# Kernel tuning notes

Measured on AMD Instinct MI355X. Metric: run time of the kernel, lower is better.

Reference implementation:

```python
import jax, jax.numpy as jnp
import numpy as np

WIN = 7
N = WIN * WIN  # 49 tokens per window
C = 384
H = 12
HD = C // H
B_ = 4096
NW = 64  # number of distinct window masks; must divide B_


def _relative_position_index(wh=WIN, ww=WIN):
    coords = np.stack(np.meshgrid(np.arange(wh), np.arange(ww), indexing='ij'))  # [2,wh,ww]
    cf = coords.reshape(2, -1)
    rel = cf[:, :, None] - cf[:, None, :]               # [2,N,N]
    rel = rel.transpose(1, 2, 0).astype(np.int32)       # [N,N,2]
    rel[:, :, 0] += wh - 1
    rel[:, :, 1] += ww - 1
    rel[:, :, 0] *= 2 * ww - 1
    return jnp.asarray(rel.sum(-1))                     # [N,N] int32


def setup_inputs() -> dict:
    key = jax.random.key(0)
    ks = jax.random.split(key, 8)
    std = 0.02
    return {
        'x': jax.random.normal(ks[0], (B_, N, C), jnp.float32),
        'mask': jnp.zeros((NW, N, N), jnp.float32),  # 0/-inf mask; zeros here
        'qkv_w': jax.random.normal(ks[1], (3 * C, C), jnp.float32) * std,
        'qkv_b': jnp.zeros((3 * C,), jnp.float32),
        'rpb_table': jax.random.normal(ks[2], ((2 * WIN - 1) ** 2, H), jnp.float32) * std,
        'proj_l_w': jax.random.normal(ks[3], (H, H), jnp.float32) * std,
        'proj_l_b': jnp.zeros((H,), jnp.float32),
        'proj_w_w': jax.random.normal(ks[4], (H, H), jnp.float32) * std,
        'proj_w_b': jnp.zeros((H,), jnp.float32),
        'proj_weight': jax.random.normal(ks[5], (C, C), jnp.float32) * std,
        'proj_bias': jnp.zeros((C,), jnp.float32),
        'rel_index': _relative_position_index(),
    }


def reference(x, mask, qkv_w, qkv_b, rpb_table, proj_l_w, proj_l_b,
              proj_w_w, proj_w_b, proj_weight, proj_bias, rel_index):
    B, n, c = x.shape
    scale = HD ** (-0.5)
    qkv = x @ qkv_w.T + qkv_b                     # [B,N,3C]
    q_out, k_out, v_out = jnp.split(qkv, 3, axis=-1)  # each [B,N,C]
    qkv5 = qkv.reshape(B, n, 3, H, HD)
    q = qkv5[:, :, 0].transpose(0, 2, 1, 3)       # [B,H,N,hd]
    k = qkv5[:, :, 1].transpose(0, 2, 1, 3)
    v = qkv5[:, :, 2].transpose(0, 2, 1, 3)
    attn = jnp.einsum('bhnd,bhmd->bhnm', q * scale, k)   # [B,H,N,N]
    bias = rpb_table[rel_index]                   # [N,N,H]
    attn = attn + bias.transpose(2, 0, 1)[None]
    # proj_l: linear mixing across heads (Linear acts on last dim after permute)
    attn = jnp.einsum('bhnm,gh->bgnm', attn, proj_l_w) + proj_l_b[None, :, None, None]
    nW = mask.shape[0]
    attn = attn.reshape(B // nW, nW, H, n, n) + mask[None, :, None]
    attn = attn.reshape(B, H, n, n)
    attn = jax.nn.softmax(attn, axis=-1)
    # proj_w: head mixing after softmax
    attn = jnp.einsum('bhnm,gh->bgnm', attn, proj_w_w) + proj_w_b[None, :, None, None]
    out = jnp.einsum('bhnm,bhmd->bnhd', attn, v).reshape(B, n, c)
    out = out @ proj_weight.T + proj_bias
    return (out, (q_out, k_out, v_out))
```

## Files before the change

### kernel.cpp

```cpp
#include <hip/hip_runtime.h>
#include <hip/hip_bf16.h>

#define TOK 49
#define NPT 2401
#define CDIM 384
#define NH 12
#define HDIM 32
#define NWIN 64
#define BTOT 4096
#define OUTSZ (BTOT * TOK * CDIM)
#define L2E 1.4426950408889634f

typedef __attribute__((ext_vector_type(8))) short bf16x8;
typedef __attribute__((ext_vector_type(4))) float f32x4;
typedef unsigned int uint32;
typedef unsigned short ushort_t;

__device__ inline ushort_t f2bf(float f) {
  uint32 u = __float_as_uint(f);
  u += 0x7FFF + ((u >> 16) & 1);
  return (ushort_t)(u >> 16);
}
__device__ inline uint32 pk2(float a, float b) {
  union { __hip_bfloat162 h; uint32 u; } x;
  x.h = __float22bfloat162_rn(float2{a, b});
  return x.u;
}
__device__ inline float bf2f(uint32 u) { return __uint_as_float((u & 0xffffu) << 16); }
__device__ inline bf16x8 pack8(float4 a, float4 b) {
  union { __hip_bfloat162 h[4]; bf16x8 v; } u;
  u.h[0] = __float22bfloat162_rn(float2{a.x, a.y});
  u.h[1] = __float22bfloat162_rn(float2{a.z, a.w});
  u.h[2] = __float22bfloat162_rn(float2{b.x, b.y});
  u.h[3] = __float22bfloat162_rn(float2{b.z, b.w});
  return u.v;
}
__device__ inline bf16x8 pack8f(const float* f) {
  union { __hip_bfloat162 h[4]; bf16x8 v; } u;
#pragma unroll
  for (int i = 0; i < 4; ++i) u.h[i] = __float22bfloat162_rn(float2{f[2*i], f[2*i+1]});
  return u.v;
}

__global__ void k_cvt(const float* __restrict__ src, ushort_t* __restrict__ dst, int n8) {
  int i = blockIdx.x * 256 + threadIdx.x;
  if (i >= n8) return;
  const float4* s = (const float4*)(src + (size_t)i * 8);
  float4 a = s[0], b = s[1];
  uint4 o;
  o.x = (uint32)f2bf(a.x) | ((uint32)f2bf(a.y) << 16);
  o.y = (uint32)f2bf(a.z) | ((uint32)f2bf(a.w) << 16);
  o.z = (uint32)f2bf(b.x) | ((uint32)f2bf(b.y) << 16);
  o.w = (uint32)f2bf(b.z) | ((uint32)f2bf(b.w) << 16);
  *(uint4*)(dst + (size_t)i * 8) = o;
}

__global__ void k_bias2(const float* __restrict__ rpb, const float* __restrict__ plw,
                        const float* __restrict__ plb, const int* __restrict__ relidx,
                        ushort_t* __restrict__ bmf) {
  int i = blockIdx.x * 256 + threadIdx.x;
  if (i >= NPT * 12) return;
  int p = i / 12, g = i - (i / 12) * 12;
  int rid = relidx[p];
  float s = plb[g];
#pragma unroll
  for (int h = 0; h < NH; ++h) s = fmaf(plw[g * NH + h], rpb[rid * NH + h], s);
  bmf[i] = f2bf(s * L2E);
}

__global__ void k_bias3(const float* __restrict__ rpb, const float* __restrict__ plw,
                        const float* __restrict__ plb, const int* __restrict__ relidx,
                        const float* __restrict__ mask, ushort_t* __restrict__ bmfw) {
  int i = blockIdx.x * 256 + threadIdx.x;
  if (i >= NWIN * NPT * 12) return;
  int w = i / (NPT * 12);
  int rem = i - w * (NPT * 12);
  int p = rem / 12, g = rem - (rem / 12) * 12;
  int rid = relidx[p];
  float s = plb[g];
#pragma unroll
  for (int h = 0; h < NH; ++h) s = fmaf(plw[g * NH + h], rpb[rid * NH + h], s);
  bmfw[i] = f2bf((s + mask[w * NPT + p]) * L2E);
}

__launch_bounds__(256)
__global__ void k_qkv_mfma(const ushort_t* __restrict__ Xb, const ushort_t* __restrict__ Wb,
                           const float* __restrict__ Bq, float* __restrict__ qslab) {
  __shared__ __align__(16) ushort_t As[128 * 64];
  __shared__ __align__(16) ushort_t Bs[128 * 64];
  const int bid = blockIdx.x;
  const int sw = (bid & 7) * 1764 + (bid >> 3);
  const int bx = sw / 9;
  const int by = sw - bx * 9;
  const int tid = threadIdx.x;
  const int l = tid & 63, l15 = l & 15, l16 = l >> 4;
  const int wv = tid >> 6;
  const int wr = wv >> 1, wc = wv & 1;
  const int row0 = bx * 128;
  const int col0 = by * 128;

  f32x4 acc[4][4];
#pragma unroll
  for (int i = 0; i < 4; ++i)
#pragma unroll
    for (int j = 0; j < 4; ++j)
#pragma unroll
      for (int e = 0; e < 4; ++e) acc[i][j][e] = 0.f;

  const int sr = tid >> 3, sc = tid & 7;
  const int sidx = (sr * 64 + sc * 8) ^ ((sr & 7) << 3);

  for (int kb = 0; kb < CDIM; kb += 64) {
#pragma unroll
    for (int i = 0; i < 4; ++i) {
      int r = sr + i * 32;
      int idx = (sidx + i * 32 * 64) ^ 0;
      uint4 v = *(const uint4*)&Xb[(size_t)(row0 + r) * CDIM + kb + sc * 8];
      *(uint4*)&As[idx] = v;
      uint4 w = *(const uint4*)&Wb[(size_t)(col0 + r) * CDIM + kb + sc * 8];
      *(uint4*)&Bs[idx] = w;
    }
    __syncthreads();
#pragma unroll
    for (int ks = 0; ks < 2; ++ks) {
      bf16x8 af[4], bfr[4];
#pragma unroll
      for (int mt = 0; mt < 4; ++mt) {
        int row = wr * 64 + mt * 16 + l15;
        af[mt] = *(const bf16x8*)&As[(row * 64 + ks * 32 + l16 * 8) ^ ((row & 7) << 3)];
      }
#pragma unroll
      for (int nt = 0; nt < 4; ++nt) {
        int row = wc * 64 + nt * 16 + l15;
        bfr[nt] = *(const bf16x8*)&Bs[(row * 64 + ks * 32 + l16 * 8) ^ ((row & 7) << 3)];
      }
#pragma unroll
      for (int mt = 0; mt < 4; ++mt)
#pragma unroll
        for (int nt = 0; nt < 4; ++nt)
          acc[mt][nt] = __builtin_amdgcn_mfma_f32_16x16x32_bf16(af[mt], bfr[nt], acc[mt][nt], 0, 0, 0);
    }
    __syncthreads();
  }

  const int slab = by / 3;
  const int cslab0 = col0 - slab * CDIM;
  float* dst = qslab + (size_t)slab * OUTSZ;
#pragma unroll
  for (int nt = 0; nt < 4; ++nt) {
    int colg = col0 + wc * 64 + nt * 16 + l15;
    int colo = cslab0 + wc * 64 + nt * 16 + l15;
    float bv = Bq[colg];
#pragma unroll
    for (int mt = 0; mt < 4; ++mt) {
      int rbase = row0 + wr * 64 + mt * 16 + l16 * 4;
#pragma unroll
      for (int j = 0; j < 4; ++j)
        dst[(size_t)(rbase + j) * CDIM + colo] = acc[mt][nt][j] + bv;
    }
  }
}

__launch_bounds__(1024, 8)
__global__ void k_attn9(const float* __restrict__ qslab, const float* __restrict__ kslab,
                        const float* __restrict__ vslab, const float* __restrict__ mask,
                        const ushort_t* __restrict__ bmf, int wstride,
                        const float* __restrict__ plw, const float* __restrict__ pww,
                        const float* __restrict__ pwb, float* __restrict__ xout) {
  __shared__ __align__(16) ushort_t SA[19976];
  __shared__ __align__(16) ushort_t PP[12 * 1400 + 416];

  const int tid = threadIdx.x;
  const int b  = blockIdx.x >> 1;
  const int bh = blockIdx.x & 1;
  const int n0 = bh * 25;
  const int NR = bh ? 24 : 25;
  const size_t base = (size_t)b * TOK * CDIM;
  const int l = tid & 63, l15 = l & 15, l16 = l >> 4;
  const int wv = tid >> 6;
  const float SCL = 0.17677669529663687f * L2E;

  for (int p = tid; p < 1240; p += 1024) *(uint2*)&SA[p * 16 + 12] = uint2{0u, 0u};
  if (tid < 580) *(uint32*)&SA[18816 + tid * 2] = 0u;
  if (tid < 208) *(uint32*)&PP[12 * 1400 + tid * 2] = 0u;

  {
    const int art = wv >> 3;
    const int act = (wv >> 1) & 3;
    const int ah0 = (wv & 1) * 6;
    const int nrow = art * 16 + l15;
    const int mrow = act * 16 + l15;
    const bool qv = nrow < NR;
    const bool kv = mrow < TOK;
#pragma unroll
    for (int hp = 0; hp < 3; ++hp) {
      f32x4 s2[2];
#pragma unroll
      for (int hh = 0; hh < 2; ++hh) {
        int h = ah0 + hp * 2 + hh;
        bf16x8 af = {0,0,0,0,0,0,0,0}, bf = {0,0,0,0,0,0,0,0};
        if (qv) {
          const float4* qp = (const float4*)(qslab + base + (size_t)(n0 + nrow) * CDIM + h * HDIM + l16 * 8);
          af = pack8(qp[0], qp[1]);
        }
        if (kv) {
          const float4* kp = (const float4*)(kslab + base + (size_t)mrow * CDIM + h * HDIM + l16 * 8);
          bf = pack8(kp[0], kp[1]);
        }
        f32x4 z = {0.f, 0.f, 0.f, 0.f};
        s2[hh] = __builtin_amdgcn_mfma_f32_16x16x32_bf16(af, bf, z, 0, 0, 0);
      }
#pragma unroll
      for (int j = 0; j < 4; ++j) {
        int nj = art * 16 + l16 * 4 + j;
        if (nj < NR && kv)
          *(uint32*)&SA[(nj * 49 + mrow) * 16 + ah0 + hp * 2] = pk2(s2[0][j], s2[1][j]);
      }
    }
  }
  __syncthreads();

  {
    const float* maskw = mask ? (mask + (size_t)(b & (NWIN - 1)) * NPT) : nullptr;
    const ushort_t* bmw = bmf + (size_t)(b & (NWIN - 1)) * wstride;
    float apf[8], bpf[8];
#pragma unroll
    for (int j = 0; j < 8; ++j) {
      int kj = l16 * 8 + j;
      apf[j] = (l15 < NH && kj < NH) ? plw[l15 * NH + kj] * SCL : 0.f;
      bpf[j] = (l15 < NH && kj < NH) ? pww[l15 * NH + kj] : 0.f;
    }
    const bf16x8 aplw = pack8f(apf);
    const bf16x8 bpww = pack8f(bpf);
    const float pwbv = (l15 < NH) ? pwb[l15] : 0.f;

    for (int nl = wv; nl < NR; nl += 16) {
      const int pb0 = nl * 49;
      float ev[4][4];
      float rs[4] = {0.f, 0.f, 0.f, 0.f};
#pragma unroll
      for (int mc = 0; mc < 4; ++mc) {
        int m = mc * 16 + l15;
        int pl = pb0 + m;
        bf16x8 sf = {0,0,0,0,0,0,0,0};
        if (l16 < 2) sf = *(const bf16x8*)&SA[pl * 16 + l16 * 8];
        int pg = pl + n0 * 49; if (pg > 2400) pg = 2400;
        uint2 bmu = *(const uint2*)&bmw[pg * 12 + l16 * 4];
        f32x4 cini = {bf2f(bmu.x), bf2f(bmu.x >> 16), bf2f(bmu.y), bf2f(bmu.y >> 16)};
        if (maskw) {
          float mk = maskw[pg] * L2E;
          cini[0] += mk; cini[1] += mk; cini[2] += mk; cini[3] += mk;
        }
        f32x4 o = __builtin_amdgcn_mfma_f32_16x16x32_bf16(aplw, sf, cini, 0, 0, 0);
        bool okm = (m < TOK);
#pragma unroll
        for (int j = 0; j < 4; ++j) {
          int g = l16 * 4 + j;
          float e = (okm && g < NH) ? exp2f(o[j]) : 0.f;
          ev[mc][j] = e;
          rs[j] += e;
        }
      }
#pragma unroll
      for (int d = 1; d < 16; d <<= 1)
#pragma unroll
        for (int j = 0; j < 4; ++j) rs[j] += __shfl_xor(rs[j], d, 64);
      float inv[4];
#pragma unroll
      for (int j = 0; j < 4; ++j) inv[j] = (rs[j] > 0.f) ? 1.f / rs[j] : 0.f;

#pragma unroll
      for (int mc = 0; mc < 4; ++mc) {
        int m = mc * 16 + l15;
        if (m < TOK) {
          uint2 w;
          w.x = pk2(ev[mc][0] * inv[0], ev[mc][1] * inv[1]);
          w.y = pk2(ev[mc][2] * inv[2], ev[mc][3] * inv[3]);
          *(uint2*)&SA[(pb0 + m) * 16 + l16 * 4] = w;
        }
      }
#pragma unroll
      for (int mc = 0; mc < 4; ++mc) {
        bf16x8 pf8 = {0,0,0,0,0,0,0,0};
        if (l16 < 2) pf8 = *(const bf16x8*)&SA[(pb0 + mc * 16 + l15) * 16 + l16 * 8];
        f32x4 cd = {pwbv, pwbv, pwbv, pwbv};
        f32x4 o = __builtin_amdgcn_mfma_f32_16x16x32_bf16(pf8, bpww, cd, 0, 0, 0);
        int m0 = mc * 16 + l16 * 4;
        if (l15 < NH && m0 < 56) {
          float z0 = (m0     < TOK) ? o[0] : 0.f;
          float z1 = (m0 + 1 < TOK) ? o[1] : 0.f;
          float z2 = (m0 + 2 < TOK) ? o[2] : 0.f;
          float z3 = (m0 + 3 < TOK) ? o[3] : 0.f;
          uint2 w;
          w.x = pk2(z0, z1);
          w.y = pk2(z2, z3);
          *(uint2*)&PP[l15 * 1400 + nl * 56 + m0] = w;
        }
      }
    }
  }
  __syncthreads();

  {
    ushort_t* Vt = SA;
    for (int i = tid; i < CDIM * 13; i += 1024) {
      int mq = i / CDIM, c = i - mq * CDIM;
      int m = mq * 4;
      float f0 = (m     < TOK) ? vslab[base + (size_t)(m    ) * CDIM + c] : 0.f;
      float f1 = (m + 1 < TOK) ? vslab[base + (size_t)(m + 1) * CDIM + c] : 0.f;
      float f2 = (m + 2 < TOK) ? vslab[base + (size_t)(m + 2) * CDIM + c] : 0.f;
      float f3 = (m + 3 < TOK) ? vslab[base + (size_t)(m + 3) * CDIM + c] : 0.f;
      uint2 u;
      u.x = pk2(f0, f1);
      u.y = pk2(f2, f3);
      *(uint2*)&Vt[c * 52 + mq * 4] = u;
    }
  }
  __syncthreads();

  {
    const ushort_t* Vt = SA;
    const int ert = wv >> 3;
    const int edt = (wv >> 2) & 1;
    const int egq = wv & 3;
#pragma unroll
    for (int gi = 0; gi < 3; ++gi) {
      int g = egq * 3 + gi;
      int col = g * HDIM + edt * 16 + l15;
      f32x4 acc = {0.f, 0.f, 0.f, 0.f};
#pragma unroll
      for (int ks = 0; ks < 2; ++ks) {
        bf16x8 pa8 = {0,0,0,0,0,0,0,0};
        bf16x8 vb8 = {0,0,0,0,0,0,0,0};
        if (!(ks == 1 && l16 == 3)) {
          pa8 = *(const bf16x8*)&PP[g * 1400 + (ert * 16 + l15) * 56 + ks * 32 + l16 * 8];
          uint2 lo = *(const uint2*)&Vt[col * 52 + ks * 32 + l16 * 8];
          uint2 hi = *(const uint2*)&Vt[col * 52 + ks * 32 + l16 * 8 + 4];
          union { uint32 u[4]; bf16x8 v; } uv;
          uv.u[0] = lo.x; uv.u[1] = lo.y; uv.u[2] = hi.x; uv.u[3] = hi.y;
          vb8 = uv.v;
        }
        acc = __builtin_amdgcn_mfma_f32_16x16x32_bf16(pa8, vb8, acc, 0, 0, 0);
      }
#pragma unroll
      for (int j = 0; j < 4; ++j) {
        int nlo = ert * 16 + l16 * 4 + j;
        if (nlo < NR)
          xout[base + (size_t)(n0 + nlo) * CDIM + col] = acc[j];
      }
    }
  }
}

__launch_bounds__(512, 4)
__global__ void k_proj3(float* __restrict__ Y, const float* __restrict__ W,
                        const float* __restrict__ Bv) {
  __shared__ __align__(16) ushort_t Asb[64 * 392];
  __shared__ __align__(16) ushort_t Bsb[384 * 40];
  const int tid = threadIdx.x;
  const int l = tid & 63, l15 = l & 15, l16 = l >> 4;
  const int wv = tid >> 6;
  const int wr = wv >> 2;
  const int wc = wv & 3;
  const int row0 = blockIdx.x * 64;

#pragma unroll
  for (int i = 0; i < 6; ++i) {
    int cid = tid + i * 512;
    int r = cid / 48, c8 = cid - (cid / 48) * 48;
    const float4* s = (const float4*)&Y[(size_t)(row0 + r) * CDIM + c8 * 8];
    float4 a = s[0], b = s[1];
    uint4 o;
    o.x = pk2(a.x, a.y); o.y = pk2(a.z, a.w);
    o.z = pk2(b.x, b.y); o.w = pk2(b.z, b.w);
    *(uint4*)&Asb[r * 392 + c8 * 8] = o;
  }

  f32x4 acc[2][6];
#pragma unroll
  for (int i = 0; i < 2; ++i)
#pragma unroll
    for (int j = 0; j < 6; ++j)
#pragma unroll
      for (int e = 0; e < 4; ++e) acc[i][j][e] = 0.f;

  for (int kb = 0; kb < 12; ++kb) {
    __syncthreads();
#pragma unroll
    for (int i = 0; i < 3; ++i) {
      int cid = tid + i * 512;
      int col = cid >> 2, k8 = cid & 3;
      const float4* s = (const float4*)&W[(size_t)col * CDIM + kb * 32 + k8 * 8];
      float4 a = s[0], b = s[1];
      uint4 o;
      o.x = pk2(a.x, a.y); o.y = pk2(a.z, a.w);
      o.z = pk2(b.x, b.y); o.w = pk2(b.z, b.w);
      *(uint4*)&Bsb[col * 40 + k8 * 8] = o;
    }
    __syncthreads();
    bf16x8 af[2], bfr[6];
#pragma unroll
    for (int mt = 0; mt < 2; ++mt)
      af[mt] = *(const bf16x8*)&Asb[(wr * 32 + mt * 16 + l15) * 392 + kb * 32 + l16 * 8];
#pragma unroll
    for (int nt = 0; nt < 6; ++nt)
      bfr[nt] = *(const bf16x8*)&Bsb[(wc * 96 + nt * 16 + l15) * 40 + l16 * 8];
#pragma unroll
    for (int mt = 0; mt < 2; ++mt)
#pragma unroll
      for (int nt = 0; nt < 6; ++nt)
        acc[mt][nt] = __builtin_amdgcn_mfma_f32_16x16x32_bf16(af[mt], bfr[nt], acc[mt][nt], 0, 0, 0);
  }

#pragma unroll
  for (int nt = 0; nt < 6; ++nt) {
    int col = wc * 96 + nt * 16 + l15;
    float bv = Bv[col];
#pragma unroll
    for (int mt = 0; mt < 2; ++mt) {
      int rbase = row0 + wr * 32 + mt * 16 + l16 * 4;
#pragma unroll
      for (int j = 0; j < 4; ++j)
        Y[(size_t)(rbase + j) * CDIM + col] = acc[mt][nt][j] + bv;
    }
  }
}

extern "C" void kernel_launch(void* const* d_in, const int* in_sizes, int n_in,
                              void* d_out, int out_size, void* d_ws, size_t ws_size,
                              hipStream_t stream) {
  const float* x      = (const float*)d_in[0];
  const float* mask   = (const float*)d_in[1];
  const float* qkv_w  = (const float*)d_in[2];
  const float* qkv_b  = (const float*)d_in[3];
  const float* rpb    = (const float*)d_in[4];
  const float* plw    = (const float*)d_in[5];
  const float* plb    = (const float*)d_in[6];
  const float* pww    = (const float*)d_in[7];
  const float* pwb    = (const float*)d_in[8];
  const float* projw  = (const float*)d_in[9];
  const float* projb  = (const float*)d_in[10];
  const int*   relidx = (const int*)d_in[11];

  float* out   = (float*)d_out;
  float* qslab = out + (size_t)OUTSZ;
  float* kslab = out + 2 * (size_t)OUTSZ;
  float* vslab = out + 3 * (size_t)OUTSZ;

  ushort_t* Xb  = (ushort_t*)out;
  ushort_t* Wb  = (ushort_t*)(out + 70000000);
  ushort_t* bmf = (ushort_t*)d_ws;

  k_cvt<<<(OUTSZ / 8 + 255) / 256, 256, 0, stream>>>(x, Xb, OUTSZ / 8);
  k_cvt<<<(3 * CDIM * CDIM / 8 + 255) / 256, 256, 0, stream>>>(qkv_w, Wb, 3 * CDIM * CDIM / 8);

  const size_t need_ws = (size_t)NWIN * NPT * 12 * sizeof(ushort_t);
  const bool folded = (ws_size >= need_ws);
  if (folded)
    k_bias3<<<(NWIN * NPT * 12 + 255) / 256, 256, 0, stream>>>(rpb, plw, plb, relidx, mask, bmf);
  else
    k_bias2<<<(NPT * 12 + 255) / 256, 256, 0, stream>>>(rpb, plw, plb, relidx, bmf);

  k_qkv_mfma<<<(BTOT * TOK / 128) * 9, 256, 0, stream>>>(Xb, Wb, qkv_b, qslab);

  k_attn9<<<BTOT * 2, 1024, 0, stream>>>(qslab, kslab, vslab,
                                         folded ? nullptr : mask, bmf,
                                         folded ? NPT * 12 : 0,
                                         plw, pww, pwb, out);

  k_proj3<<<BTOT * TOK / 64, 512, 0, stream>>>(out, projw, projb);
}
```

Baseline: 1.319 ms.

## Fuse X bf16 conversion into QKV GEMM with full-row X tile in LDS

Removes the separate kernel that converted X from fp32 to bf16. The QKV GEMM now reads fp32 X directly, converts it while staging a 64-row by full-K tile into LDS, and loops over all 9 output column blocks so each X tile is loaded once. Weight fragments are read straight from global memory (L2-resident) rather than staged in LDS. This saves a full pass writing and re-reading X, at the cost of a larger LDS footprint per block, no double buffering, and weight loads that are not coalesced through shared memory.

Result: faster. 1.246 ms (-5.5%).

```diff
diff --git a/kernel.cpp b/kernel.cpp
--- a/kernel.cpp
+++ b/kernel.cpp
@@ -84,79 +84,69 @@
 }
 
 __launch_bounds__(256)
-__global__ void k_qkv_mfma(const ushort_t* __restrict__ Xb, const ushort_t* __restrict__ Wb,
+__global__ void k_qkv_mega(const float* __restrict__ X, const ushort_t* __restrict__ Wb,
                            const float* __restrict__ Bq, float* __restrict__ qslab) {
-  __shared__ __align__(16) ushort_t As[128 * 64];
-  __shared__ __align__(16) ushort_t Bs[128 * 64];
+  __shared__ __align__(16) ushort_t Xs[64 * 392];
   const int bid = blockIdx.x;
-  const int sw = (bid & 7) * 1764 + (bid >> 3);
-  const int bx = sw / 9;
-  const int by = sw - bx * 9;
+  const int sw = (bid & 7) * 392 + (bid >> 3);
+  const int row0 = sw * 64;
   const int tid = threadIdx.x;
   const int l = tid & 63, l15 = l & 15, l16 = l >> 4;
-  const int wv = tid >> 6;
-  const int wr = wv >> 1, wc = wv & 1;
-  const int row0 = bx * 128;
-  const int col0 = by * 128;
-
-  f32x4 acc[4][4];
-#pragma unroll
-  for (int i = 0; i < 4; ++i)
-#pragma unroll
-    for (int j = 0; j < 4; ++j)
-#pragma unroll
-      for (int e = 0; e < 4; ++e) acc[i][j][e] = 0.f;
-
-  const int sr = tid >> 3, sc = tid & 7;
-  const int sidx = (sr * 64 + sc * 8) ^ ((sr & 7) << 3);
-
-  for (int kb = 0; kb < CDIM; kb += 64) {
-#pragma unroll
-    for (int i = 0; i < 4; ++i) {
-      int r = sr + i * 32;
-      int idx = (sidx + i * 32 * 64) ^ 0;
-      uint4 v = *(const uint4*)&Xb[(size_t)(row0 + r) * CDIM + kb + sc * 8];
-      *(uint4*)&As[idx] = v;
-      uint4 w = *(const uint4*)&Wb[(size_t)(col0 + r) * CDIM + kb + sc * 8];
-      *(uint4*)&Bs[idx] = w;
-    }
-    __syncthreads();
-#pragma unroll
-    for (int ks = 0; ks < 2; ++ks) {
-      bf16x8 af[4], bfr[4];
+  const int wc = tid >> 6;
+
+#pragma unroll
+  for (int i = 0; i < 12; ++i) {
+    int cid = tid + i * 256;
+    int r = cid / 48, c8 = cid - (cid / 48) * 48;
+    const float4* s = (const float4*)&X[(size_t)(row0 + r) * CDIM + c8 * 8];
+    float4 a = s[0], b = s[1];
+    uint4 o;
+    o.x = pk2(a.x, a.y); o.y = pk2(a.z, a.w);
+    o.z = pk2(b.x, b.y); o.w = pk2(b.z, b.w);
+    *(uint4*)&Xs[r * 392 + c8 * 8] = o;
+  }
+  __syncthreads();
+
+  for (int by = 0; by < 9; ++by) {
+    f32x4 acc[4][2];
+#pragma unroll
+    for (int mt = 0; mt < 4; ++mt)
+#pragma unroll
+      for (int nt = 0; nt < 2; ++nt)
+#pragma unroll
+        for (int e = 0; e < 4; ++e) acc[mt][nt][e] = 0.f;
+
+#pragma unroll 2
+    for (int ks = 0; ks < 12; ++ks) {
+      bf16x8 af[4], bfr[2];
+#pragma unroll
+      for (int mt = 0; mt < 4; ++mt)
+        af[mt] = *(const bf16x8*)&Xs[(mt * 16 + l15) * 392 + ks * 32 + l16 * 8];
+#pragma unroll
+      for (int nt = 0; nt < 2; ++nt)
+        bfr[nt] = *(const bf16x8*)&Wb[(size_t)(by * 128 + wc * 32 + nt * 16 + l15) * CDIM + ks * 32 + l16 * 8];
+#pragma unroll
+      for (int mt = 0; mt < 4; ++mt)
+#pragma unroll
+        for (int nt = 0; nt < 2; ++nt)
+          acc[mt][nt] = __builtin_amdgcn_mfma_f32_16x16x32_bf16(af[mt], bfr[nt], acc[mt][nt], 0, 0, 0);
+    }
+
+    const int slab = by / 3;
+    const int cbase = (by - slab * 3) * 128;
+    float* dst = qslab + (size_t)slab * OUTSZ;
+#pragma unroll
+    for (int nt = 0; nt < 2; ++nt) {
+      int colg = by * 128 + wc * 32 + nt * 16 + l15;
+      int colo = cbase + wc * 32 + nt * 16 + l15;
+      float bv = Bq[colg];
 #pragma unroll
       for (int mt = 0; mt < 4; ++mt) {
-        int row = wr * 64 + mt * 16 + l15;
-        af[mt] = *(const bf16x8*)&As[(row * 64 + ks * 32 + l16 * 8) ^ ((row & 7) << 3)];
-      }
-#pragma unroll
-      for (int nt = 0; nt < 4; ++nt) {
-        int row = wc * 64 + nt * 16 + l15;
-        bfr[nt] = *(const bf16x8*)&Bs[(row * 64 + ks * 32 + l16 * 8) ^ ((row & 7) << 3)];
-      }
-#pragma unroll
-      for (int mt = 0; mt < 4; ++mt)
-#pragma unroll
-        for (int nt = 0; nt < 4; ++nt)
-          acc[mt][nt] = __builtin_amdgcn_mfma_f32_16x16x32_bf16(af[mt], bfr[nt], acc[mt][nt], 0, 0, 0);
-    }
-    __syncthreads();
-  }
-
-  const int slab = by / 3;
-  const int cslab0 = col0 - slab * CDIM;
-  float* dst = qslab + (size_t)slab * OUTSZ;
-#pragma unroll
-  for (int nt = 0; nt < 4; ++nt) {
-    int colg = col0 + wc * 64 + nt * 16 + l15;
-    int colo = cslab0 + wc * 64 + nt * 16 + l15;
-    float bv = Bq[colg];
-#pragma unroll
-    for (int mt = 0; mt < 4; ++mt) {
-      int rbase = row0 + wr * 64 + mt * 16 + l16 * 4;
-#pragma unroll
-      for (int j = 0; j < 4; ++j)
-        dst[(size_t)(rbase + j) * CDIM + colo] = acc[mt][nt][j] + bv;
+        int rbase = row0 + mt * 16 + l16 * 4;
+#pragma unroll
+        for (int j = 0; j < 4; ++j)
+          dst[(size_t)(rbase + j) * CDIM + colo] = acc[mt][nt][j] + bv;
+      }
     }
   }
 }
@@ -447,11 +437,9 @@
   float* kslab = out + 2 * (size_t)OUTSZ;
   float* vslab = out + 3 * (size_t)OUTSZ;
 
-  ushort_t* Xb  = (ushort_t*)out;
   ushort_t* Wb  = (ushort_t*)(out + 70000000);
   ushort_t* bmf = (ushort_t*)d_ws;
 
-  k_cvt<<<(OUTSZ / 8 + 255) / 256, 256, 0, stream>>>(x, Xb, OUTSZ / 8);
   k_cvt<<<(3 * CDIM * CDIM / 8 + 255) / 256, 256, 0, stream>>>(qkv_w, Wb, 3 * CDIM * CDIM / 8);
 
   const size_t need_ws = (size_t)NWIN * NPT * 12 * sizeof(ushort_t);
@@ -461,7 +449,7 @@
   else
     k_bias2<<<(NPT * 12 + 255) / 256, 256, 0, stream>>>(rpb, plw, plb, relidx, bmf);
 
-  k_qkv_mfma<<<(BTOT * TOK / 128) * 9, 256, 0, stream>>>(Xb, Wb, qkv_b, qslab);
+  k_qkv_mega<<<BTOT * TOK / 64, 256, 0, stream>>>(x, Wb, qkv_b, qslab);
 
   k_attn9<<<BTOT * 2, 1024, 0, stream>>>(qslab, kslab, vslab,
                                          folded ? nullptr : mask, bmf,
```
